# Optimization experiments

Hardware: AMD Instinct MI355X
Metric: run time of the kernel (lower is better)

The kernel has to match this reference:

```python
import jax, jax.numpy as jnp
import numpy as np

TOP_K = 4


def setup_inputs() -> dict:
    key = jax.random.key(0)
    ks = jax.random.split(key, 6)
    B, S, H, I, E = 2, 2048, 2880, 2880, 8
    scale = 0.02
    return {
        "x": jax.random.normal(ks[0], (B, S, H), dtype=jnp.float32),
        "router_w": jax.random.normal(ks[1], (E, H), dtype=jnp.float32) * scale,
        "router_b": jax.random.normal(ks[2], (E,), dtype=jnp.float32) * scale,
        "w_gate": jax.random.normal(ks[3], (E, H, I), dtype=jnp.float32) * scale,
        "w_up": jax.random.normal(ks[4], (E, H, I), dtype=jnp.float32) * scale,
        "w_down": jax.random.normal(ks[5], (E, I, H), dtype=jnp.float32) * scale,
    }


def _moe_forward(x, router_w, router_b, w_gate, w_up, w_down):
    B, S, H = x.shape
    E = router_w.shape[0]
    xf = x.reshape(-1, H)  # (T, H); note: self.norm is unused in the original forward
    T = xf.shape[0]

    # Router: linear -> top-k -> softmax over the k selected logits
    logits = xf @ router_w.T + router_b          # (T, E)
    topv, topi = jax.lax.top_k(logits, TOP_K)    # (T, K)
    aff_k = jax.nn.softmax(topv, axis=-1)        # (T, K), sums to 1
    aff = jnp.zeros_like(logits).at[jnp.arange(T)[:, None], topi].set(aff_k)  # (T, E)

    # Expert SwiGLU MLPs, affinity-weighted combine (aff is 0 for unselected experts)
    out = jnp.zeros_like(xf)
    for e in range(E):  # fixed small structural loop over experts
        g = xf @ w_gate[e]                       # (T, I)
        u = xf @ w_up[e]                         # (T, I)
        h = jax.nn.silu(g) * u                   # SwiGLU
        out = out + aff[:, e:e + 1] * (h @ w_down[e])
    return out.reshape(B, S, H)


def reference(x, router_w, router_b, w_gate, w_up, w_down):
    return _moe_forward(x, router_w, router_b, w_gate, w_up, w_down)
```

## Files before the change

### kernel.cpp

```cpp
#include <hip/hip_runtime.h>

#define T_TOK 4096
#define HDIM  2880
#define IDIM  2880
#define NEXP  8
#define TOPK  4
#define WEL   (2880 * 2880)

#define BM 128
#define BN 96
#define BK 64
#define NSTEP 45

typedef __attribute__((ext_vector_type(8))) short  s16x8;
typedef __attribute__((ext_vector_type(8))) unsigned short u16x8;
typedef __attribute__((ext_vector_type(4))) float  f32x4;

__device__ __forceinline__ unsigned short f2bf(float f) {
  unsigned int u = __float_as_uint(f);
  u += 0x7FFFu + ((u >> 16) & 1u);
  return (unsigned short)(u >> 16);
}

__device__ __forceinline__ void gload16(const unsigned short* g, unsigned short* l) {
  __builtin_amdgcn_global_load_lds(
      (const __attribute__((address_space(1))) void*)g,
      (__attribute__((address_space(3))) void*)l, 16, 0, 0);
}

__global__ __launch_bounds__(256) void cvt_kernel(const float* __restrict__ x,
                                                  unsigned short* __restrict__ xb) {
  int i = blockIdx.x * 256 + threadIdx.x;
  const f32x4* p = (const f32x4*)x;
  f32x4 a = p[2 * (size_t)i];
  f32x4 b = p[2 * (size_t)i + 1];
  u16x8 o;
  o[0] = f2bf(a[0]); o[1] = f2bf(a[1]); o[2] = f2bf(a[2]); o[3] = f2bf(a[3]);
  o[4] = f2bf(b[0]); o[5] = f2bf(b[1]); o[6] = f2bf(b[2]); o[7] = f2bf(b[3]);
  *(u16x8*)(xb + (size_t)i * 8) = o;
}

__global__ __launch_bounds__(256) void transpose_group_kernel(
    const float* __restrict__ wg, const float* __restrict__ wu,
    const float* __restrict__ wd, unsigned short* __restrict__ wbuf, int ge) {
  __shared__ unsigned short st[64][72];
  const int z = blockIdx.z, j = z / 3, m = z % 3;
  const float* src = (m == 0 ? wg : (m == 1 ? wu : wd)) + (size_t)(ge + j) * WEL;
  unsigned short* dst = wbuf + (size_t)(j * 3 + m) * WEL;
  const int k0 = blockIdx.x * 64, n0 = blockIdx.y * 64;
  const int tid = threadIdx.x;
#pragma unroll
  for (int u = 0; u < 4; ++u) {
    int idx = tid + u * 256;
    int kr = idx >> 4;
    int nc = (idx & 15) * 4;
    f32x4 v = *(const f32x4*)(src + (size_t)(k0 + kr) * 2880 + (n0 + nc));
#pragma unroll
    for (int q = 0; q < 4; ++q) st[nc + q][kr] = f2bf(v[q]);
  }
  __syncthreads();
  int n = tid >> 2;
  int kc = (tid & 3) * 16;
  u16x8 a = *(const u16x8*)(&st[n][kc]);
  u16x8 b = *(const u16x8*)(&st[n][kc + 8]);
  unsigned short* po = dst + (size_t)(n0 + n) * 2880 + (k0 + kc);
  *(u16x8*)(po) = a;
  *(u16x8*)(po + 8) = b;
}

__global__ __launch_bounds__(256) void router_kernel(const float* __restrict__ x,
                                                     const float* __restrict__ rw,
                                                     const float* __restrict__ rb,
                                                     float* __restrict__ aff,
                                                     int* __restrict__ cnt,
                                                     int* __restrict__ lst) {
  const int wv = threadIdx.x >> 6, lane = threadIdx.x & 63;
  const int tok0 = (blockIdx.x * 4 + wv) * 4;
  float acc[4][NEXP];
#pragma unroll
  for (int t = 0; t < 4; ++t)
#pragma unroll
    for (int e = 0; e < NEXP; ++e) acc[t][e] = 0.f;

#pragma unroll
  for (int it = 0; it < 12; ++it) {
    int c = it * 64 + lane;
    if (c < 720) {
      f32x4 w4[NEXP];
#pragma unroll
      for (int e = 0; e < NEXP; ++e)
        w4[e] = *(const f32x4*)(rw + (size_t)e * HDIM + c * 4);
#pragma unroll
      for (int t = 0; t < 4; ++t) {
        f32x4 xv = *(const f32x4*)(x + (size_t)(tok0 + t) * HDIM + c * 4);
#pragma unroll
        for (int e = 0; e < NEXP; ++e)
          acc[t][e] += xv[0] * w4[e][0] + xv[1] * w4[e][1] + xv[2] * w4[e][2] + xv[3] * w4[e][3];
      }
    }
  }
#pragma unroll
  for (int t = 0; t < 4; ++t)
#pragma unroll
    for (int e = 0; e < NEXP; ++e) {
#pragma unroll
      for (int m = 32; m; m >>= 1) acc[t][e] += __shfl_xor(acc[t][e], m);
    }
  if (lane < 4) {
    int tok = tok0 + lane;
    float lg[NEXP];
#pragma unroll
    for (int e = 0; e < NEXP; ++e) lg[e] = acc[lane][e] + rb[e];
    bool used[NEXP];
#pragma unroll
    for (int e = 0; e < NEXP; ++e) used[e] = false;
    int bi[TOPK]; float bv[TOPK];
#pragma unroll
    for (int s = 0; s < TOPK; ++s) {
      int best = 0; float vbest = -1e30f;
#pragma unroll
      for (int e = 0; e < NEXP; ++e)
        if (!used[e] && lg[e] > vbest) { vbest = lg[e]; best = e; }
      used[best] = true; bi[s] = best; bv[s] = vbest;
    }
    float mx = bv[0];
    float w[TOPK]; float ssum = 0.f;
#pragma unroll
    for (int s = 0; s < TOPK; ++s) { w[s] = __expf(bv[s] - mx); ssum += w[s]; }
    float o[NEXP];
#pragma unroll
    for (int e = 0; e < NEXP; ++e) o[e] = 0.f;
#pragma unroll
    for (int s = 0; s < TOPK; ++s) o[bi[s]] = w[s] / ssum;
#pragma unroll
    for (int e = 0; e < NEXP; ++e) aff[(size_t)tok * NEXP + e] = o[e];
#pragma unroll
    for (int s = 0; s < TOPK; ++s) {
      int p = atomicAdd(&cnt[bi[s]], 1);
      lst[bi[s] * T_TOK + p] = tok;
    }
  }
}

__global__ void sched_kernel(const int* __restrict__ cnt, int* __restrict__ ebs,
                             int* __restrict__ ess, int* __restrict__ gtot, int G) {
  if (threadIdx.x == 0 && blockIdx.x == 0) {
    int ng = NEXP / G;
    for (int g = 0; g < ng; ++g) {
      int b = 0, s = 0;
      for (int j = 0; j < G; ++j) {
        int e = g * G + j;
        ebs[e] = b; ess[e] = s;
        b += (cnt[e] + BM - 1) / BM;
        s += cnt[e];
      }
      gtot[g] = b;
    }
  }
}

__global__ __launch_bounds__(256) void gateup_kernel(
    const unsigned short* __restrict__ xb, const unsigned short* __restrict__ wbuf,
    const float* __restrict__ aff, const int* __restrict__ lst,
    const int* __restrict__ cnts, const int* __restrict__ ebs,
    const int* __restrict__ ess, const int* __restrict__ gtot_g,
    unsigned short* __restrict__ h4, int ge, int G) {
  const int bx = blockIdx.x;
  if (bx >= *gtot_g) return;
  int j = 0;
  for (int t = 1; t < G; ++t) j += (bx >= ebs[ge + t]) ? 1 : 0;
  const int e = ge + j;
  const int cnt = cnts[e];
  const int m0 = (bx - ebs[e]) * BM;
  const int slotbase = ess[e];
  const unsigned short* wgt = wbuf + (size_t)j * 3 * WEL;
  const unsigned short* wut = wgt + WEL;

  __shared__ __align__(16) unsigned short Al[BM * BK];
  __shared__ __align__(16) unsigned short Bgl[BN * BK];
  __shared__ __align__(16) unsigned short Bul[BN * BK];

  const int tid = threadIdx.x;
  const int n0 = blockIdx.y * BN;
  const int wv = tid >> 6, lane = tid & 63;
  const int msub = (wv >> 1) * 64, nsub = (wv & 1) * 48;
  const int l15 = lane & 15, l4 = lane >> 4;
  const int lr = lane >> 3, lc = lane & 7;
  const int* mylst = lst + e * T_TOK;

  const unsigned short* asrc[4]; unsigned short* adst[4];
#pragma unroll
  for (int u = 0; u < 4; ++u) {
    int s = u * 4 + wv;
    int r = s * 8 + lr;
    int tok = mylst[min(m0 + r, cnt - 1)];
    asrc[u] = xb + (size_t)tok * HDIM + (lc ^ (r & 7)) * 8;
    adst[u] = &Al[s * 512];
  }
  const unsigned short* bgsrc[3]; const unsigned short* busrc[3];
  unsigned short* bgdst[3]; unsigned short* budst[3];
#pragma unroll
  for (int u = 0; u < 3; ++u) {
    int s = u * 4 + wv;
    int r = s * 8 + lr;
    size_t off = (size_t)(n0 + r) * HDIM + (size_t)((lc ^ (r & 7)) * 8);
    bgsrc[u] = wgt + off; busrc[u] = wut + off;
    bgdst[u] = &Bgl[s * 512]; budst[u] = &Bul[s * 512];
  }

  f32x4 accg[4][3]; f32x4 accu[4][3];
#pragma unroll
  for (int mf = 0; mf < 4; ++mf)
#pragma unroll
    for (int nf = 0; nf < 3; ++nf) { accg[mf][nf] = (f32x4)0.f; accu[mf][nf] = (f32x4)0.f; }

#pragma unroll 1
  for (int k0 = 0; k0 < HDIM; k0 += BK) {
#pragma unroll
    for (int u = 0; u < 4; ++u) gload16(asrc[u] + k0, adst[u]);
#pragma unroll
    for (int u = 0; u < 3; ++u) {
      gload16(bgsrc[u] + k0, bgdst[u]);
      gload16(busrc[u] + k0, budst[u]);
    }
    __syncthreads();
#pragma unroll
    for (int kk = 0; kk < 2; ++kk) {
      s16x8 af[4];
#pragma unroll
      for (int mf = 0; mf < 4; ++mf) {
        int R = msub + mf * 16 + l15;
        int sl = (kk * 4 + l4) ^ (R & 7);
        af[mf] = *(const s16x8*)(&Al[R * 64 + sl * 8]);
      }
#pragma unroll
      for (int nf = 0; nf < 3; ++nf) {
        int R = nsub + nf * 16 + l15;
        int sl = (kk * 4 + l4) ^ (R & 7);
        s16x8 bg = *(const s16x8*)(&Bgl[R * 64 + sl * 8]);
        s16x8 bu = *(const s16x8*)(&Bul[R * 64 + sl * 8]);
#pragma unroll
        for (int mf = 0; mf < 4; ++mf) {
          accg[mf][nf] = __builtin_amdgcn_mfma_f32_16x16x32_bf16(af[mf], bg, accg[mf][nf], 0, 0, 0);
          accu[mf][nf] = __builtin_amdgcn_mfma_f32_16x16x32_bf16(af[mf], bu, accu[mf][nf], 0, 0, 0);
        }
      }
    }
    __syncthreads();
  }

#pragma unroll
  for (int mf = 0; mf < 4; ++mf)
#pragma unroll
    for (int r = 0; r < 4; ++r) {
      int slot = m0 + msub + mf * 16 + l4 * 4 + r;
      if (slot < cnt) {
        int tok = mylst[slot];
        float av = aff[(size_t)tok * NEXP + e];
#pragma unroll
        for (int nf = 0; nf < 3; ++nf) {
          float g = accg[mf][nf][r], uu = accu[mf][nf][r];
          float hv = (g / (1.f + __expf(-g))) * uu * av;
          int col = n0 + nsub + nf * 16 + l15;
          h4[(size_t)(slotbase + slot) * IDIM + col] = f2bf(hv);
        }
      }
    }
}

__global__ __launch_bounds__(256) void down_kernel(
    const unsigned short* __restrict__ h4, const unsigned short* __restrict__ wbuf,
    float* __restrict__ out, const int* __restrict__ lst,
    const int* __restrict__ cnts, const int* __restrict__ ebs,
    const int* __restrict__ ess, const int* __restrict__ gtot_g,
    int ge, int G) {
  const int bx = blockIdx.x;
  if (bx >= *gtot_g) return;
  int j = 0;
  for (int t = 1; t < G; ++t) j += (bx >= ebs[ge + t]) ? 1 : 0;
  const int e = ge + j;
  const int cnt = cnts[e];
  const int m0 = (bx - ebs[e]) * BM;
  const int slotbase = ess[e];
  const unsigned short* wdt = wbuf + (size_t)j * 3 * WEL + 2 * (size_t)WEL;

  __shared__ __align__(16) unsigned short Al[BM * BK];
  __shared__ __align__(16) unsigned short Bl[BN * BK];

  const int tid = threadIdx.x;
  const int n0 = blockIdx.y * BN;
  const int wv = tid >> 6, lane = tid & 63;
  const int msub = (wv >> 1) * 64, nsub = (wv & 1) * 48;
  const int l15 = lane & 15, l4 = lane >> 4;
  const int lr = lane >> 3, lc = lane & 7;
  const int* mylst = lst + e * T_TOK;

  const unsigned short* asrc[4]; unsigned short* adst[4];
#pragma unroll
  for (int u = 0; u < 4; ++u) {
    int s = u * 4 + wv;
    int r = s * 8 + lr;
    int hr = min(m0 + r, cnt - 1);
    asrc[u] = h4 + (size_t)(slotbase + hr) * IDIM + (lc ^ (r & 7)) * 8;
    adst[u] = &Al[s * 512];
  }
  const unsigned short* bsrc[3]; unsigned short* bdst[3];
#pragma unroll
  for (int u = 0; u < 3; ++u) {
    int s = u * 4 + wv;
    int r = s * 8 + lr;
    bsrc[u] = wdt + (size_t)(n0 + r) * IDIM + (size_t)((lc ^ (r & 7)) * 8);
    bdst[u] = &Bl[s * 512];
  }

  f32x4 acc[4][3];
#pragma unroll
  for (int mf = 0; mf < 4; ++mf)
#pragma unroll
    for (int nf = 0; nf < 3; ++nf) acc[mf][nf] = (f32x4)0.f;

#pragma unroll 1
  for (int k0 = 0; k0 < IDIM; k0 += BK) {
#pragma unroll
    for (int u = 0; u < 4; ++u) gload16(asrc[u] + k0, adst[u]);
#pragma unroll
    for (int u = 0; u < 3; ++u) gload16(bsrc[u] + k0, bdst[u]);
    __syncthreads();
#pragma unroll
    for (int kk = 0; kk < 2; ++kk) {
      s16x8 af[4];
#pragma unroll
      for (int mf = 0; mf < 4; ++mf) {
        int R = msub + mf * 16 + l15;
        int sl = (kk * 4 + l4) ^ (R & 7);
        af[mf] = *(const s16x8*)(&Al[R * 64 + sl * 8]);
      }
#pragma unroll
      for (int nf = 0; nf < 3; ++nf) {
        int R = nsub + nf * 16 + l15;
        int sl = (kk * 4 + l4) ^ (R & 7);
        s16x8 bb = *(const s16x8*)(&Bl[R * 64 + sl * 8]);
#pragma unroll
        for (int mf = 0; mf < 4; ++mf)
          acc[mf][nf] = __builtin_amdgcn_mfma_f32_16x16x32_bf16(af[mf], bb, acc[mf][nf], 0, 0, 0);
      }
    }
    __syncthreads();
  }

#pragma unroll
  for (int mf = 0; mf < 4; ++mf)
#pragma unroll
    for (int r = 0; r < 4; ++r) {
      int slot = m0 + msub + mf * 16 + l4 * 4 + r;
      if (slot < cnt) {
        int tok = mylst[slot];
#pragma unroll
        for (int nf = 0; nf < 3; ++nf) {
          int col = n0 + nsub + nf * 16 + l15;
          atomicAdd(out + (size_t)tok * HDIM + col, acc[mf][nf][r]);
        }
      }
    }
}

extern "C" void kernel_launch(void* const* d_in, const int* in_sizes, int n_in,
                              void* d_out, int out_size, void* d_ws, size_t ws_size,
                              hipStream_t stream) {
  (void)in_sizes; (void)n_in;
  const float* x  = (const float*)d_in[0];
  const float* rw = (const float*)d_in[1];
  const float* rb = (const float*)d_in[2];
  const float* wg = (const float*)d_in[3];
  const float* wu = (const float*)d_in[4];
  const float* wd = (const float*)d_in[5];
  float* out = (float*)d_out;

  char* ws = (char*)d_ws;
  float* aff = (float*)ws;
  int*   cnt = (int*)(ws + 131072);
  int*   lst = (int*)(ws + 131584);
  int*   ebs = (int*)(ws + 262656);
  int*   ess = (int*)(ws + 262720);
  int*   gtot = (int*)(ws + 262784);
  unsigned short* xb = (unsigned short*)(ws + 263168);
  const size_t OFF_H4 = 263168 + 23592960ull;

  const size_t WELB = (size_t)WEL * 2;
  int G = 1;
  {
    size_t need8 = OFF_H4 + (size_t)16384 * IDIM * 2 + 8 * 3 * WELB;
    size_t need2 = OFF_H4 + (size_t)8192  * IDIM * 2 + 2 * 3 * WELB;
    if (ws_size >= need8) G = 8;
    else if (ws_size >= need2) G = 2;
  }
  const size_t h4b = (size_t)((G == 8) ? 16384 : (G == 2 ? 8192 : 4096)) * IDIM * 2;
  unsigned short* h4   = (unsigned short*)(ws + OFF_H4);
  unsigned short* wbuf = (unsigned short*)(ws + OFF_H4 + h4b);

  const int NG = NEXP / G;
  const int GUX = (G == 8) ? 136 : (G == 2 ? 66 : 33);

  hipMemsetAsync(out, 0, (size_t)out_size * sizeof(float), stream);
  hipMemsetAsync(cnt, 0, 512, stream);
  cvt_kernel<<<(T_TOK * HDIM / 8) / 256, 256, 0, stream>>>(x, xb);
  router_kernel<<<T_TOK / 16, 256, 0, stream>>>(x, rw, rb, aff, cnt, lst);
  sched_kernel<<<1, 64, 0, stream>>>(cnt, ebs, ess, gtot, G);

  for (int g = 0; g < NG; ++g) {
    int ge = g * G;
    transpose_group_kernel<<<dim3(45, 45, 3 * G), 256, 0, stream>>>(wg, wu, wd, wbuf, ge);
    gateup_kernel<<<dim3(GUX, IDIM / BN), 256, 0, stream>>>(
        xb, wbuf, aff, lst, cnt, ebs, ess, gtot + g, h4, ge, G);
    down_kernel<<<dim3(GUX, HDIM / BN), 256, 0, stream>>>(
        h4, wbuf, out, lst, cnt, ebs, ess, gtot + g, ge, G);
  }
}
```

Before: 1.463 ms.

## Double-buffer LDS tiles in expert GEMMs and flatten grid to 1D panels

Both expert GEMM kernels now use two LDS buffers. The next K-tile's global-to-LDS loads are issued before computing on the current tile, with partial vmcnt waits instead of full syncthreads, so memory latency overlaps MFMA work. The 2D grid is also replaced by a 1D grid in which a block index maps to an (expert, m-tile, n-panel) triple, with m varying fastest inside each n panel. This is meant to compact out unused blocks and improve weight-panel reuse in cache. It doubles LDS use per block, which can lower occupancy, and it relies on hand-counted vmcnt values being correct.

```diff
diff --git a/kernel.cpp b/kernel.cpp
--- a/kernel.cpp
+++ b/kernel.cpp
@@ -10,6 +10,9 @@
 #define BM 128
 #define BN 96
 #define BK 64
+#define NPAN 30
+#define ASZ (BM * BK)
+#define BSZ (BN * BK)
 #define NSTEP 45
 
 typedef __attribute__((ext_vector_type(8))) short  s16x8;
@@ -142,7 +145,7 @@
   }
 }
 
-__global__ void sched_kernel(const int* __restrict__ cnt, int* __restrict__ ebs,
+__global__ void sched_kernel(const int* __restrict__ cnt, int* __restrict__ gbs,
                              int* __restrict__ ess, int* __restrict__ gtot, int G) {
   if (threadIdx.x == 0 && blockIdx.x == 0) {
     int ng = NEXP / G;
@@ -150,38 +153,50 @@
       int b = 0, s = 0;
       for (int j = 0; j < G; ++j) {
         int e = g * G + j;
-        ebs[e] = b; ess[e] = s;
-        b += (cnt[e] + BM - 1) / BM;
+        gbs[e] = b; ess[e] = s;
+        b += ((cnt[e] + BM - 1) / BM) * NPAN;
         s += cnt[e];
       }
       gtot[g] = b;
     }
   }
+}
+
+__device__ __forceinline__ bool locate(int bx, const int* gbs, const int* cnts,
+                                       int ge, int G, const int* gtot_g,
+                                       int& e, int& m0, int& n0, int& cnt) {
+  if (bx >= *gtot_g) return false;
+  int j = 0;
+  for (int t = 1; t < G; ++t) j += (bx >= gbs[ge + t]) ? 1 : 0;
+  e = ge + j;
+  cnt = cnts[e];
+  int mb = (cnt + BM - 1) >> 7;
+  int local = bx - gbs[e];
+  int nIdx = local / mb;
+  int mIdx = local - nIdx * mb;
+  m0 = mIdx * BM;
+  n0 = nIdx * BN;
+  return true;
 }
 
 __global__ __launch_bounds__(256) void gateup_kernel(
     const unsigned short* __restrict__ xb, const unsigned short* __restrict__ wbuf,
     const float* __restrict__ aff, const int* __restrict__ lst,
-    const int* __restrict__ cnts, const int* __restrict__ ebs,
+    const int* __restrict__ cnts, const int* __restrict__ gbs,
     const int* __restrict__ ess, const int* __restrict__ gtot_g,
     unsigned short* __restrict__ h4, int ge, int G) {
-  const int bx = blockIdx.x;
-  if (bx >= *gtot_g) return;
-  int j = 0;
-  for (int t = 1; t < G; ++t) j += (bx >= ebs[ge + t]) ? 1 : 0;
-  const int e = ge + j;
-  const int cnt = cnts[e];
-  const int m0 = (bx - ebs[e]) * BM;
+  int e, m0, n0, cnt;
+  if (!locate(blockIdx.x, gbs, cnts, ge, G, gtot_g, e, m0, n0, cnt)) return;
+  const int j = e - ge;
   const int slotbase = ess[e];
   const unsigned short* wgt = wbuf + (size_t)j * 3 * WEL;
   const unsigned short* wut = wgt + WEL;
 
-  __shared__ __align__(16) unsigned short Al[BM * BK];
-  __shared__ __align__(16) unsigned short Bgl[BN * BK];
-  __shared__ __align__(16) unsigned short Bul[BN * BK];
+  __shared__ __align__(16) unsigned short Al[2 * ASZ];
+  __shared__ __align__(16) unsigned short Bgl[2 * BSZ];
+  __shared__ __align__(16) unsigned short Bul[2 * BSZ];
 
   const int tid = threadIdx.x;
-  const int n0 = blockIdx.y * BN;
   const int wv = tid >> 6, lane = tid & 63;
   const int msub = (wv >> 1) * 64, nsub = (wv & 1) * 48;
   const int l15 = lane & 15, l4 = lane >> 4;
@@ -214,16 +229,20 @@
 #pragma unroll
     for (int nf = 0; nf < 3; ++nf) { accg[mf][nf] = (f32x4)0.f; accu[mf][nf] = (f32x4)0.f; }
 
-#pragma unroll 1
-  for (int k0 = 0; k0 < HDIM; k0 += BK) {
-#pragma unroll
-    for (int u = 0; u < 4; ++u) gload16(asrc[u] + k0, adst[u]);
+  auto stage = [&](int buf, int k0) {
+    int ao = buf * ASZ, bo = buf * BSZ;
+#pragma unroll
+    for (int u = 0; u < 4; ++u) gload16(asrc[u] + k0, adst[u] + ao);
 #pragma unroll
     for (int u = 0; u < 3; ++u) {
-      gload16(bgsrc[u] + k0, bgdst[u]);
-      gload16(busrc[u] + k0, budst[u]);
-    }
-    __syncthreads();
+      gload16(bgsrc[u] + k0, bgdst[u] + bo);
+      gload16(busrc[u] + k0, budst[u] + bo);
+    }
+  };
+  auto compute = [&](int buf) {
+    const unsigned short* Ab = Al + buf * ASZ;
+    const unsigned short* Bg = Bgl + buf * BSZ;
+    const unsigned short* Bu = Bul + buf * BSZ;
 #pragma unroll
     for (int kk = 0; kk < 2; ++kk) {
       s16x8 af[4];
@@ -231,14 +250,14 @@
       for (int mf = 0; mf < 4; ++mf) {
         int R = msub + mf * 16 + l15;
         int sl = (kk * 4 + l4) ^ (R & 7);
-        af[mf] = *(const s16x8*)(&Al[R * 64 + sl * 8]);
+        af[mf] = *(const s16x8*)(&Ab[R * 64 + sl * 8]);
       }
 #pragma unroll
       for (int nf = 0; nf < 3; ++nf) {
         int R = nsub + nf * 16 + l15;
         int sl = (kk * 4 + l4) ^ (R & 7);
-        s16x8 bg = *(const s16x8*)(&Bgl[R * 64 + sl * 8]);
-        s16x8 bu = *(const s16x8*)(&Bul[R * 64 + sl * 8]);
+        s16x8 bg = *(const s16x8*)(&Bg[R * 64 + sl * 8]);
+        s16x8 bu = *(const s16x8*)(&Bu[R * 64 + sl * 8]);
 #pragma unroll
         for (int mf = 0; mf < 4; ++mf) {
           accg[mf][nf] = __builtin_amdgcn_mfma_f32_16x16x32_bf16(af[mf], bg, accg[mf][nf], 0, 0, 0);
@@ -246,8 +265,25 @@
         }
       }
     }
-    __syncthreads();
-  }
+  };
+
+  stage(0, 0);
+#pragma unroll 1
+  for (int t = 0; t < NSTEP - 1; t += 2) {
+    stage(1, (t + 1) * BK);
+    asm volatile("s_waitcnt vmcnt(10)" ::: "memory");
+    __builtin_amdgcn_s_barrier();
+    compute(0);
+    __builtin_amdgcn_s_barrier();
+    stage(0, (t + 2) * BK);
+    asm volatile("s_waitcnt vmcnt(10)" ::: "memory");
+    __builtin_amdgcn_s_barrier();
+    compute(1);
+    __builtin_amdgcn_s_barrier();
+  }
+  asm volatile("s_waitcnt vmcnt(0)" ::: "memory");
+  __builtin_amdgcn_s_barrier();
+  compute(0);
 
 #pragma unroll
   for (int mf = 0; mf < 4; ++mf)
@@ -271,24 +307,19 @@
 __global__ __launch_bounds__(256) void down_kernel(
     const unsigned short* __restrict__ h4, const unsigned short* __restrict__ wbuf,
     float* __restrict__ out, const int* __restrict__ lst,
-    const int* __restrict__ cnts, const int* __restrict__ ebs,
+    const int* __restrict__ cnts, const int* __restrict__ gbs,
     const int* __restrict__ ess, const int* __restrict__ gtot_g,
     int ge, int G) {
-  const int bx = blockIdx.x;
-  if (bx >= *gtot_g) return;
-  int j = 0;
-  for (int t = 1; t < G; ++t) j += (bx >= ebs[ge + t]) ? 1 : 0;
-  const int e = ge + j;
-  const int cnt = cnts[e];
-  const int m0 = (bx - ebs[e]) * BM;
+  int e, m0, n0, cnt;
+  if (!locate(blockIdx.x, gbs, cnts, ge, G, gtot_g, e, m0, n0, cnt)) return;
+  const int j = e - ge;
   const int slotbase = ess[e];
   const unsigned short* wdt = wbuf + (size_t)j * 3 * WEL + 2 * (size_t)WEL;
 
-  __shared__ __align__(16) unsigned short Al[BM * BK];
-  __shared__ __align__(16) unsigned short Bl[BN * BK];
+  __shared__ __align__(16) unsigned short Al[2 * ASZ];
+  __shared__ __align__(16) unsigned short Bl[2 * BSZ];
 
   const int tid = threadIdx.x;
-  const int n0 = blockIdx.y * BN;
   const int wv = tid >> 6, lane = tid & 63;
   const int msub = (wv >> 1) * 64, nsub = (wv & 1) * 48;
   const int l15 = lane & 15, l4 = lane >> 4;
@@ -319,13 +350,16 @@
 #pragma unroll
     for (int nf = 0; nf < 3; ++nf) acc[mf][nf] = (f32x4)0.f;
 
-#pragma unroll 1
-  for (int k0 = 0; k0 < IDIM; k0 += BK) {
-#pragma unroll
-    for (int u = 0; u < 4; ++u) gload16(asrc[u] + k0, adst[u]);
-#pragma unroll
-    for (int u = 0; u < 3; ++u) gload16(bsrc[u] + k0, bdst[u]);
-    __syncthreads();
+  auto stage = [&](int buf, int k0) {
+    int ao = buf * ASZ, bo = buf * BSZ;
+#pragma unroll
+    for (int u = 0; u < 4; ++u) gload16(asrc[u] + k0, adst[u] + ao);
+#pragma unroll
+    for (int u = 0; u < 3; ++u) gload16(bsrc[u] + k0, bdst[u] + bo);
+  };
+  auto compute = [&](int buf) {
+    const unsigned short* Ab = Al + buf * ASZ;
+    const unsigned short* Bb = Bl + buf * BSZ;
 #pragma unroll
     for (int kk = 0; kk < 2; ++kk) {
       s16x8 af[4];
@@ -333,20 +367,37 @@
       for (int mf = 0; mf < 4; ++mf) {
         int R = msub + mf * 16 + l15;
         int sl = (kk * 4 + l4) ^ (R & 7);
-        af[mf] = *(const s16x8*)(&Al[R * 64 + sl * 8]);
+        af[mf] = *(const s16x8*)(&Ab[R * 64 + sl * 8]);
       }
 #pragma unroll
       for (int nf = 0; nf < 3; ++nf) {
         int R = nsub + nf * 16 + l15;
         int sl = (kk * 4 + l4) ^ (R & 7);
-        s16x8 bb = *(const s16x8*)(&Bl[R * 64 + sl * 8]);
+        s16x8 bb = *(const s16x8*)(&Bb[R * 64 + sl * 8]);
 #pragma unroll
         for (int mf = 0; mf < 4; ++mf)
           acc[mf][nf] = __builtin_amdgcn_mfma_f32_16x16x32_bf16(af[mf], bb, acc[mf][nf], 0, 0, 0);
       }
     }
-    __syncthreads();
-  }
+  };
+
+  stage(0, 0);
+#pragma unroll 1
+  for (int t = 0; t < NSTEP - 1; t += 2) {
+    stage(1, (t + 1) * BK);
+    asm volatile("s_waitcnt vmcnt(7)" ::: "memory");
+    __builtin_amdgcn_s_barrier();
+    compute(0);
+    __builtin_amdgcn_s_barrier();
+    stage(0, (t + 2) * BK);
+    asm volatile("s_waitcnt vmcnt(7)" ::: "memory");
+    __builtin_amdgcn_s_barrier();
+    compute(1);
+    __builtin_amdgcn_s_barrier();
+  }
+  asm volatile("s_waitcnt vmcnt(0)" ::: "memory");
+  __builtin_amdgcn_s_barrier();
+  compute(0);
 
 #pragma unroll
   for (int mf = 0; mf < 4; ++mf)
@@ -380,7 +431,7 @@
   float* aff = (float*)ws;
   int*   cnt = (int*)(ws + 131072);
   int*   lst = (int*)(ws + 131584);
-  int*   ebs = (int*)(ws + 262656);
+  int*   gbs = (int*)(ws + 262656);
   int*   ess = (int*)(ws + 262720);
   int*   gtot = (int*)(ws + 262784);
   unsigned short* xb = (unsigned short*)(ws + 263168);
@@ -399,20 +450,20 @@
   unsigned short* wbuf = (unsigned short*)(ws + OFF_H4 + h4b);
 
   const int NG = NEXP / G;
-  const int GUX = (G == 8) ? 136 : (G == 2 ? 66 : 33);
+  const int NBLK = (128 + G) * NPAN;
 
   hipMemsetAsync(out, 0, (size_t)out_size * sizeof(float), stream);
   hipMemsetAsync(cnt, 0, 512, stream);
   cvt_kernel<<<(T_TOK * HDIM / 8) / 256, 256, 0, stream>>>(x, xb);
   router_kernel<<<T_TOK / 16, 256, 0, stream>>>(x, rw, rb, aff, cnt, lst);
-  sched_kernel<<<1, 64, 0, stream>>>(cnt, ebs, ess, gtot, G);
+  sched_kernel<<<1, 64, 0, stream>>>(cnt, gbs, ess, gtot, G);
 
   for (int g = 0; g < NG; ++g) {
     int ge = g * G;
     transpose_group_kernel<<<dim3(45, 45, 3 * G), 256, 0, stream>>>(wg, wu, wd, wbuf, ge);
-    gateup_kernel<<<dim3(GUX, IDIM / BN), 256, 0, stream>>>(
-        xb, wbuf, aff, lst, cnt, ebs, ess, gtot + g, h4, ge, G);
-    down_kernel<<<dim3(GUX, HDIM / BN), 256, 0, stream>>>(
-        h4, wbuf, out, lst, cnt, ebs, ess, gtot + g, ge, G);
-  }
-}
+    gateup_kernel<<<NBLK, 256, 0, stream>>>(
+        xb, wbuf, aff, lst, cnt, gbs, ess, gtot + g, h4, ge, G);
+    down_kernel<<<NBLK, 256, 0, stream>>>(
+        h4, wbuf, out, lst, cnt, gbs, ess, gtot + g, ge, G);
+  }
+}
```

Result: faster. 1.410 ms (-3.6%).

## Double-buffer LDS with staged prefetch, 512-thread 256-row tiles, flattened XCD-swizzled grid

Applied to the files above, without the earlier changes.

Both expert GEMM kernels now use double-buffered LDS. Global-to-LDS prefetches for the next K step are split across barrier-separated MFMA phases, with s_setprio raised around the MFMA bursts. Tiles grow to 256 rows and 512 threads, the down kernel's N tile doubles to 192, and the 2D grid becomes a 1D flattened grid remapped through an XCD-aware swizzle so neighbouring tiles share L2. The goal is to hide load latency and improve operand reuse, at the cost of much more LDS and register use per block, lower occupancy, and a more fragile hand-written waitcnt schedule.

```diff
diff --git a/kernel.cpp b/kernel.cpp
--- a/kernel.cpp
+++ b/kernel.cpp
@@ -7,9 +7,15 @@
 #define TOPK  4
 #define WEL   (2880 * 2880)
 
-#define BM 128
-#define BN 96
+#define BM 256
+#define BN_GU 96
+#define BN_DN 192
 #define BK 64
+#define NPAN_GU 30
+#define NPAN_DN 15
+#define ASZ (BM * BK)
+#define BSZ_GU (BN_GU * BK)
+#define BSZ_DN (BN_DN * BK)
 #define NSTEP 45
 
 typedef __attribute__((ext_vector_type(8))) short  s16x8;
@@ -26,6 +32,12 @@
   __builtin_amdgcn_global_load_lds(
       (const __attribute__((address_space(1))) void*)g,
       (__attribute__((address_space(3))) void*)l, 16, 0, 0);
+}
+
+__device__ __forceinline__ int xcd_swz(int orig, int n) {
+  int q = n >> 3, r = n & 7;
+  int x = orig & 7, idx = orig >> 3;
+  return (x < r ? x * (q + 1) : r * (q + 1) + (x - r) * q) + idx;
 }
 
 __global__ __launch_bounds__(256) void cvt_kernel(const float* __restrict__ x,
@@ -142,46 +154,53 @@
   }
 }
 
-__global__ void sched_kernel(const int* __restrict__ cnt, int* __restrict__ ebs,
-                             int* __restrict__ ess, int* __restrict__ gtot, int G) {
+__global__ void sched_kernel(const int* __restrict__ cnt, int* __restrict__ gbs_gu,
+                             int* __restrict__ gbs_dn, int* __restrict__ ess,
+                             int* __restrict__ gtot_gu, int* __restrict__ gtot_dn, int G) {
   if (threadIdx.x == 0 && blockIdx.x == 0) {
     int ng = NEXP / G;
     for (int g = 0; g < ng; ++g) {
-      int b = 0, s = 0;
+      int bg_ = 0, bd_ = 0, s = 0;
       for (int j = 0; j < G; ++j) {
         int e = g * G + j;
-        ebs[e] = b; ess[e] = s;
-        b += (cnt[e] + BM - 1) / BM;
+        gbs_gu[e] = bg_; gbs_dn[e] = bd_; ess[e] = s;
+        int mb = (cnt[e] + BM - 1) / BM;
+        bg_ += mb * NPAN_GU;
+        bd_ += mb * NPAN_DN;
         s += cnt[e];
       }
-      gtot[g] = b;
-    }
-  }
-}
-
-__global__ __launch_bounds__(256) void gateup_kernel(
+      gtot_gu[g] = bg_; gtot_dn[g] = bd_;
+    }
+  }
+}
+
+__global__ __launch_bounds__(512) void gateup_kernel(
     const unsigned short* __restrict__ xb, const unsigned short* __restrict__ wbuf,
     const float* __restrict__ aff, const int* __restrict__ lst,
-    const int* __restrict__ cnts, const int* __restrict__ ebs,
+    const int* __restrict__ cnts, const int* __restrict__ gbs,
     const int* __restrict__ ess, const int* __restrict__ gtot_g,
     unsigned short* __restrict__ h4, int ge, int G) {
-  const int bx = blockIdx.x;
-  if (bx >= *gtot_g) return;
+  const int gt = *gtot_g;
+  if ((int)blockIdx.x >= gt) return;
+  const int bx = xcd_swz(blockIdx.x, gt);
   int j = 0;
-  for (int t = 1; t < G; ++t) j += (bx >= ebs[ge + t]) ? 1 : 0;
+  for (int t = 1; t < G; ++t) j += (bx >= gbs[ge + t]) ? 1 : 0;
   const int e = ge + j;
   const int cnt = cnts[e];
-  const int m0 = (bx - ebs[e]) * BM;
+  const int mb = (cnt + BM - 1) >> 8;
+  const int local = bx - gbs[e];
+  const int nIdx = local / mb;
+  const int m0 = (local - nIdx * mb) * BM;
+  const int n0 = nIdx * BN_GU;
   const int slotbase = ess[e];
   const unsigned short* wgt = wbuf + (size_t)j * 3 * WEL;
   const unsigned short* wut = wgt + WEL;
 
-  __shared__ __align__(16) unsigned short Al[BM * BK];
-  __shared__ __align__(16) unsigned short Bgl[BN * BK];
-  __shared__ __align__(16) unsigned short Bul[BN * BK];
+  __shared__ __align__(16) unsigned short Al[2 * ASZ];
+  __shared__ __align__(16) unsigned short Bgl[2 * BSZ_GU];
+  __shared__ __align__(16) unsigned short Bul[2 * BSZ_GU];
 
   const int tid = threadIdx.x;
-  const int n0 = blockIdx.y * BN;
   const int wv = tid >> 6, lane = tid & 63;
   const int msub = (wv >> 1) * 64, nsub = (wv & 1) * 48;
   const int l15 = lane & 15, l4 = lane >> 4;
@@ -191,21 +210,26 @@
   const unsigned short* asrc[4]; unsigned short* adst[4];
 #pragma unroll
   for (int u = 0; u < 4; ++u) {
-    int s = u * 4 + wv;
+    int s = wv + 8 * u;
     int r = s * 8 + lr;
     int tok = mylst[min(m0 + r, cnt - 1)];
     asrc[u] = xb + (size_t)tok * HDIM + (lc ^ (r & 7)) * 8;
     adst[u] = &Al[s * 512];
   }
-  const unsigned short* bgsrc[3]; const unsigned short* busrc[3];
-  unsigned short* bgdst[3]; unsigned short* budst[3];
-#pragma unroll
-  for (int u = 0; u < 3; ++u) {
-    int s = u * 4 + wv;
-    int r = s * 8 + lr;
-    size_t off = (size_t)(n0 + r) * HDIM + (size_t)((lc ^ (r & 7)) * 8);
-    bgsrc[u] = wgt + off; busrc[u] = wut + off;
-    bgdst[u] = &Bgl[s * 512]; budst[u] = &Bul[s * 512];
+  const unsigned short* bsrc[3]; unsigned short* bdst[3];
+  {
+    int r0 = wv * 8 + lr;
+    bsrc[0] = wgt + (size_t)(n0 + r0) * HDIM + (size_t)((lc ^ (r0 & 7)) * 8);
+    bdst[0] = &Bgl[wv * 512];
+    int s1 = (wv < 4) ? (8 + wv) : wv;
+    int r1 = s1 * 8 + lr;
+    size_t o1 = (size_t)(n0 + r1) * HDIM + (size_t)((lc ^ (r1 & 7)) * 8);
+    bsrc[1] = (wv < 4) ? (wgt + o1) : (wut + o1);
+    bdst[1] = (wv < 4) ? &Bgl[s1 * 512] : &Bul[s1 * 512];
+    int s2 = (wv < 4) ? wv : (4 + wv);
+    int r2 = s2 * 8 + lr;
+    bsrc[2] = wut + (size_t)(n0 + r2) * HDIM + (size_t)((lc ^ (r2 & 7)) * 8);
+    bdst[2] = &Bul[s2 * 512];
   }
 
   f32x4 accg[4][3]; f32x4 accu[4][3];
@@ -214,39 +238,89 @@
 #pragma unroll
     for (int nf = 0; nf < 3; ++nf) { accg[mf][nf] = (f32x4)0.f; accu[mf][nf] = (f32x4)0.f; }
 
+  gload16(asrc[0], adst[0]); gload16(asrc[1], adst[1]); gload16(asrc[2], adst[2]);
+  gload16(asrc[3], adst[3]);
+  gload16(bsrc[0], bdst[0]); gload16(bsrc[1], bdst[1]); gload16(bsrc[2], bdst[2]);
+
 #pragma unroll 1
-  for (int k0 = 0; k0 < HDIM; k0 += BK) {
-#pragma unroll
-    for (int u = 0; u < 4; ++u) gload16(asrc[u] + k0, adst[u]);
-#pragma unroll
-    for (int u = 0; u < 3; ++u) {
-      gload16(bgsrc[u] + k0, bgdst[u]);
-      gload16(busrc[u] + k0, budst[u]);
-    }
-    __syncthreads();
-#pragma unroll
-    for (int kk = 0; kk < 2; ++kk) {
-      s16x8 af[4];
-#pragma unroll
-      for (int mf = 0; mf < 4; ++mf) {
-        int R = msub + mf * 16 + l15;
-        int sl = (kk * 4 + l4) ^ (R & 7);
-        af[mf] = *(const s16x8*)(&Al[R * 64 + sl * 8]);
-      }
-#pragma unroll
-      for (int nf = 0; nf < 3; ++nf) {
-        int R = nsub + nf * 16 + l15;
-        int sl = (kk * 4 + l4) ^ (R & 7);
-        s16x8 bg = *(const s16x8*)(&Bgl[R * 64 + sl * 8]);
-        s16x8 bu = *(const s16x8*)(&Bul[R * 64 + sl * 8]);
-#pragma unroll
-        for (int mf = 0; mf < 4; ++mf) {
-          accg[mf][nf] = __builtin_amdgcn_mfma_f32_16x16x32_bf16(af[mf], bg, accg[mf][nf], 0, 0, 0);
-          accu[mf][nf] = __builtin_amdgcn_mfma_f32_16x16x32_bf16(af[mf], bu, accu[mf][nf], 0, 0, 0);
-        }
-      }
-    }
-    __syncthreads();
+  for (int t = 0; t < NSTEP; ++t) {
+    const int buf = t & 1, nb = buf ^ 1;
+    const int k1 = (t + 1) * BK;
+    const unsigned short* Ab = Al + buf * ASZ;
+    const unsigned short* Bg = Bgl + buf * BSZ_GU;
+    const unsigned short* Bu = Bul + buf * BSZ_GU;
+    if (t + 1 < NSTEP) {
+      gload16(asrc[0] + k1, adst[0] + nb * ASZ);
+      gload16(asrc[1] + k1, adst[1] + nb * ASZ);
+      gload16(asrc[2] + k1, adst[2] + nb * ASZ);
+      asm volatile("s_waitcnt vmcnt(3)" ::: "memory");
+    } else {
+      asm volatile("s_waitcnt vmcnt(0)" ::: "memory");
+    }
+    __builtin_amdgcn_s_barrier();
+    s16x8 af[4];
+#pragma unroll
+    for (int mf = 0; mf < 4; ++mf) {
+      int R = msub + mf * 16 + l15;
+      af[mf] = *(const s16x8*)(&Ab[R * 64 + (l4 ^ (R & 7)) * 8]);
+    }
+    __builtin_amdgcn_s_setprio(1);
+#pragma unroll
+    for (int nf = 0; nf < 3; ++nf) {
+      int R = nsub + nf * 16 + l15;
+      s16x8 b = *(const s16x8*)(&Bg[R * 64 + (l4 ^ (R & 7)) * 8]);
+#pragma unroll
+      for (int mf = 0; mf < 4; ++mf)
+        accg[mf][nf] = __builtin_amdgcn_mfma_f32_16x16x32_bf16(af[mf], b, accg[mf][nf], 0, 0, 0);
+    }
+    __builtin_amdgcn_s_setprio(0);
+    if (t + 1 < NSTEP) {
+      gload16(asrc[3] + k1, adst[3] + nb * ASZ);
+      gload16(bsrc[0] + k1, bdst[0] + nb * BSZ_GU);
+    }
+    __builtin_amdgcn_s_barrier();
+    __builtin_amdgcn_s_setprio(1);
+#pragma unroll
+    for (int nf = 0; nf < 3; ++nf) {
+      int R = nsub + nf * 16 + l15;
+      s16x8 b = *(const s16x8*)(&Bu[R * 64 + (l4 ^ (R & 7)) * 8]);
+#pragma unroll
+      for (int mf = 0; mf < 4; ++mf)
+        accu[mf][nf] = __builtin_amdgcn_mfma_f32_16x16x32_bf16(af[mf], b, accu[mf][nf], 0, 0, 0);
+    }
+    __builtin_amdgcn_s_setprio(0);
+    if (t + 1 < NSTEP) {
+      gload16(bsrc[1] + k1, bdst[1] + nb * BSZ_GU);
+      gload16(bsrc[2] + k1, bdst[2] + nb * BSZ_GU);
+    }
+    __builtin_amdgcn_s_barrier();
+#pragma unroll
+    for (int mf = 0; mf < 4; ++mf) {
+      int R = msub + mf * 16 + l15;
+      af[mf] = *(const s16x8*)(&Ab[R * 64 + ((4 + l4) ^ (R & 7)) * 8]);
+    }
+    __builtin_amdgcn_s_setprio(1);
+#pragma unroll
+    for (int nf = 0; nf < 3; ++nf) {
+      int R = nsub + nf * 16 + l15;
+      s16x8 b = *(const s16x8*)(&Bg[R * 64 + ((4 + l4) ^ (R & 7)) * 8]);
+#pragma unroll
+      for (int mf = 0; mf < 4; ++mf)
+        accg[mf][nf] = __builtin_amdgcn_mfma_f32_16x16x32_bf16(af[mf], b, accg[mf][nf], 0, 0, 0);
+    }
+    __builtin_amdgcn_s_setprio(0);
+    __builtin_amdgcn_s_barrier();
+    __builtin_amdgcn_s_setprio(1);
+#pragma unroll
+    for (int nf = 0; nf < 3; ++nf) {
+      int R = nsub + nf * 16 + l15;
+      s16x8 b = *(const s16x8*)(&Bu[R * 64 + ((4 + l4) ^ (R & 7)) * 8]);
+#pragma unroll
+      for (int mf = 0; mf < 4; ++mf)
+        accu[mf][nf] = __builtin_amdgcn_mfma_f32_16x16x32_bf16(af[mf], b, accu[mf][nf], 0, 0, 0);
+    }
+    __builtin_amdgcn_s_setprio(0);
+    __builtin_amdgcn_s_barrier();
   }
 
 #pragma unroll
@@ -268,29 +342,33 @@
     }
 }
 
-__global__ __launch_bounds__(256) void down_kernel(
+__global__ __launch_bounds__(512) void down_kernel(
     const unsigned short* __restrict__ h4, const unsigned short* __restrict__ wbuf,
     float* __restrict__ out, const int* __restrict__ lst,
-    const int* __restrict__ cnts, const int* __restrict__ ebs,
+    const int* __restrict__ cnts, const int* __restrict__ gbs,
     const int* __restrict__ ess, const int* __restrict__ gtot_g,
     int ge, int G) {
-  const int bx = blockIdx.x;
-  if (bx >= *gtot_g) return;
+  const int gt = *gtot_g;
+  if ((int)blockIdx.x >= gt) return;
+  const int bx = xcd_swz(blockIdx.x, gt);
   int j = 0;
-  for (int t = 1; t < G; ++t) j += (bx >= ebs[ge + t]) ? 1 : 0;
+  for (int t = 1; t < G; ++t) j += (bx >= gbs[ge + t]) ? 1 : 0;
   const int e = ge + j;
   const int cnt = cnts[e];
-  const int m0 = (bx - ebs[e]) * BM;
+  const int mb = (cnt + BM - 1) >> 8;
+  const int local = bx - gbs[e];
+  const int nIdx = local / mb;
+  const int m0 = (local - nIdx * mb) * BM;
+  const int n0 = nIdx * BN_DN;
   const int slotbase = ess[e];
   const unsigned short* wdt = wbuf + (size_t)j * 3 * WEL + 2 * (size_t)WEL;
 
-  __shared__ __align__(16) unsigned short Al[BM * BK];
-  __shared__ __align__(16) unsigned short Bl[BN * BK];
+  __shared__ __align__(16) unsigned short Al[2 * ASZ];
+  __shared__ __align__(16) unsigned short Bl[2 * BSZ_DN];
 
   const int tid = threadIdx.x;
-  const int n0 = blockIdx.y * BN;
   const int wv = tid >> 6, lane = tid & 63;
-  const int msub = (wv >> 1) * 64, nsub = (wv & 1) * 48;
+  const int msub = (wv >> 1) * 64, nsub = (wv & 1) * 96;
   const int l15 = lane & 15, l4 = lane >> 4;
   const int lr = lane >> 3, lc = lane & 7;
   const int* mylst = lst + e * T_TOK;
@@ -298,7 +376,7 @@
   const unsigned short* asrc[4]; unsigned short* adst[4];
 #pragma unroll
   for (int u = 0; u < 4; ++u) {
-    int s = u * 4 + wv;
+    int s = wv + 8 * u;
     int r = s * 8 + lr;
     int hr = min(m0 + r, cnt - 1);
     asrc[u] = h4 + (size_t)(slotbase + hr) * IDIM + (lc ^ (r & 7)) * 8;
@@ -306,46 +384,101 @@
   }
   const unsigned short* bsrc[3]; unsigned short* bdst[3];
 #pragma unroll
-  for (int u = 0; u < 3; ++u) {
-    int s = u * 4 + wv;
+  for (int v = 0; v < 3; ++v) {
+    int s = wv + 8 * v;
     int r = s * 8 + lr;
-    bsrc[u] = wdt + (size_t)(n0 + r) * IDIM + (size_t)((lc ^ (r & 7)) * 8);
-    bdst[u] = &Bl[s * 512];
-  }
-
-  f32x4 acc[4][3];
+    bsrc[v] = wdt + (size_t)(n0 + r) * IDIM + (size_t)((lc ^ (r & 7)) * 8);
+    bdst[v] = &Bl[s * 512];
+  }
+
+  f32x4 acc[4][6];
 #pragma unroll
   for (int mf = 0; mf < 4; ++mf)
 #pragma unroll
-    for (int nf = 0; nf < 3; ++nf) acc[mf][nf] = (f32x4)0.f;
+    for (int nf = 0; nf < 6; ++nf) acc[mf][nf] = (f32x4)0.f;
+
+  gload16(asrc[0], adst[0]); gload16(asrc[1], adst[1]); gload16(asrc[2], adst[2]);
+  gload16(asrc[3], adst[3]);
+  gload16(bsrc[0], bdst[0]); gload16(bsrc[1], bdst[1]); gload16(bsrc[2], bdst[2]);
 
 #pragma unroll 1
-  for (int k0 = 0; k0 < IDIM; k0 += BK) {
-#pragma unroll
-    for (int u = 0; u < 4; ++u) gload16(asrc[u] + k0, adst[u]);
-#pragma unroll
-    for (int u = 0; u < 3; ++u) gload16(bsrc[u] + k0, bdst[u]);
-    __syncthreads();
-#pragma unroll
-    for (int kk = 0; kk < 2; ++kk) {
-      s16x8 af[4];
-#pragma unroll
-      for (int mf = 0; mf < 4; ++mf) {
-        int R = msub + mf * 16 + l15;
-        int sl = (kk * 4 + l4) ^ (R & 7);
-        af[mf] = *(const s16x8*)(&Al[R * 64 + sl * 8]);
-      }
-#pragma unroll
-      for (int nf = 0; nf < 3; ++nf) {
-        int R = nsub + nf * 16 + l15;
-        int sl = (kk * 4 + l4) ^ (R & 7);
-        s16x8 bb = *(const s16x8*)(&Bl[R * 64 + sl * 8]);
-#pragma unroll
-        for (int mf = 0; mf < 4; ++mf)
-          acc[mf][nf] = __builtin_amdgcn_mfma_f32_16x16x32_bf16(af[mf], bb, acc[mf][nf], 0, 0, 0);
-      }
-    }
-    __syncthreads();
+  for (int t = 0; t < NSTEP; ++t) {
+    const int buf = t & 1, nb = buf ^ 1;
+    const int k1 = (t + 1) * BK;
+    const unsigned short* Ab = Al + buf * ASZ;
+    const unsigned short* Bb = Bl + buf * BSZ_DN;
+    if (t + 1 < NSTEP) {
+      gload16(asrc[0] + k1, adst[0] + nb * ASZ);
+      gload16(asrc[1] + k1, adst[1] + nb * ASZ);
+      gload16(asrc[2] + k1, adst[2] + nb * ASZ);
+      asm volatile("s_waitcnt vmcnt(3)" ::: "memory");
+    } else {
+      asm volatile("s_waitcnt vmcnt(0)" ::: "memory");
+    }
+    __builtin_amdgcn_s_barrier();
+    s16x8 af[4];
+#pragma unroll
+    for (int mf = 0; mf < 4; ++mf) {
+      int R = msub + mf * 16 + l15;
+      af[mf] = *(const s16x8*)(&Ab[R * 64 + (l4 ^ (R & 7)) * 8]);
+    }
+    __builtin_amdgcn_s_setprio(1);
+#pragma unroll
+    for (int nf = 0; nf < 3; ++nf) {
+      int R = nsub + nf * 16 + l15;
+      s16x8 b = *(const s16x8*)(&Bb[R * 64 + (l4 ^ (R & 7)) * 8]);
+#pragma unroll
+      for (int mf = 0; mf < 4; ++mf)
+        acc[mf][nf] = __builtin_amdgcn_mfma_f32_16x16x32_bf16(af[mf], b, acc[mf][nf], 0, 0, 0);
+    }
+    __builtin_amdgcn_s_setprio(0);
+    if (t + 1 < NSTEP) {
+      gload16(asrc[3] + k1, adst[3] + nb * ASZ);
+      gload16(bsrc[0] + k1, bdst[0] + nb * BSZ_DN);
+    }
+    __builtin_amdgcn_s_barrier();
+    __builtin_amdgcn_s_setprio(1);
+#pragma unroll
+    for (int nf = 3; nf < 6; ++nf) {
+      int R = nsub + nf * 16 + l15;
+      s16x8 b = *(const s16x8*)(&Bb[R * 64 + (l4 ^ (R & 7)) * 8]);
+#pragma unroll
+      for (int mf = 0; mf < 4; ++mf)
+        acc[mf][nf] = __builtin_amdgcn_mfma_f32_16x16x32_bf16(af[mf], b, acc[mf][nf], 0, 0, 0);
+    }
+    __builtin_amdgcn_s_setprio(0);
+    if (t + 1 < NSTEP) {
+      gload16(bsrc[1] + k1, bdst[1] + nb * BSZ_DN);
+      gload16(bsrc[2] + k1, bdst[2] + nb * BSZ_DN);
+    }
+    __builtin_amdgcn_s_barrier();
+#pragma unroll
+    for (int mf = 0; mf < 4; ++mf) {
+      int R = msub + mf * 16 + l15;
+      af[mf] = *(const s16x8*)(&Ab[R * 64 + ((4 + l4) ^ (R & 7)) * 8]);
+    }
+    __builtin_amdgcn_s_setprio(1);
+#pragma unroll
+    for (int nf = 0; nf < 3; ++nf) {
+      int R = nsub + nf * 16 + l15;
+      s16x8 b = *(const s16x8*)(&Bb[R * 64 + ((4 + l4) ^ (R & 7)) * 8]);
+#pragma unroll
+      for (int mf = 0; mf < 4; ++mf)
+        acc[mf][nf] = __builtin_amdgcn_mfma_f32_16x16x32_bf16(af[mf], b, acc[mf][nf], 0, 0, 0);
+    }
+    __builtin_amdgcn_s_setprio(0);
+    __builtin_amdgcn_s_barrier();
+    __builtin_amdgcn_s_setprio(1);
+#pragma unroll
+    for (int nf = 3; nf < 6; ++nf) {
+      int R = nsub + nf * 16 + l15;
+      s16x8 b = *(const s16x8*)(&Bb[R * 64 + ((4 + l4) ^ (R & 7)) * 8]);
+#pragma unroll
+      for (int mf = 0; mf < 4; ++mf)
+        acc[mf][nf] = __builtin_amdgcn_mfma_f32_16x16x32_bf16(af[mf], b, acc[mf][nf], 0, 0, 0);
+    }
+    __builtin_amdgcn_s_setprio(0);
+    __builtin_amdgcn_s_barrier();
   }
 
 #pragma unroll
@@ -356,7 +489,7 @@
       if (slot < cnt) {
         int tok = mylst[slot];
 #pragma unroll
-        for (int nf = 0; nf < 3; ++nf) {
+        for (int nf = 0; nf < 6; ++nf) {
           int col = n0 + nsub + nf * 16 + l15;
           atomicAdd(out + (size_t)tok * HDIM + col, acc[mf][nf][r]);
         }
@@ -377,12 +510,14 @@
   float* out = (float*)d_out;
 
   char* ws = (char*)d_ws;
-  float* aff = (float*)ws;
-  int*   cnt = (int*)(ws + 131072);
-  int*   lst = (int*)(ws + 131584);
-  int*   ebs = (int*)(ws + 262656);
-  int*   ess = (int*)(ws + 262720);
-  int*   gtot = (int*)(ws + 262784);
+  float* aff     = (float*)ws;
+  int*   cnt     = (int*)(ws + 131072);
+  int*   lst     = (int*)(ws + 131584);
+  int*   gbs_gu  = (int*)(ws + 262656);
+  int*   gbs_dn  = (int*)(ws + 262720);
+  int*   ess     = (int*)(ws + 262784);
+  int*   gtot_gu = (int*)(ws + 262848);
+  int*   gtot_dn = (int*)(ws + 262912);
   unsigned short* xb = (unsigned short*)(ws + 263168);
   const size_t OFF_H4 = 263168 + 23592960ull;
 
@@ -399,20 +534,21 @@
   unsigned short* wbuf = (unsigned short*)(ws + OFF_H4 + h4b);
 
   const int NG = NEXP / G;
-  const int GUX = (G == 8) ? 136 : (G == 2 ? 66 : 33);
+  const int NBLK_GU = (T_TOK * TOPK / BM + NEXP) * NPAN_GU;
+  const int NBLK_DN = (T_TOK * TOPK / BM + NEXP) * NPAN_DN;
 
   hipMemsetAsync(out, 0, (size_t)out_size * sizeof(float), stream);
   hipMemsetAsync(cnt, 0, 512, stream);
   cvt_kernel<<<(T_TOK * HDIM / 8) / 256, 256, 0, stream>>>(x, xb);
   router_kernel<<<T_TOK / 16, 256, 0, stream>>>(x, rw, rb, aff, cnt, lst);
-  sched_kernel<<<1, 64, 0, stream>>>(cnt, ebs, ess, gtot, G);
+  sched_kernel<<<1, 64, 0, stream>>>(cnt, gbs_gu, gbs_dn, ess, gtot_gu, gtot_dn, G);
 
   for (int g = 0; g < NG; ++g) {
     int ge = g * G;
     transpose_group_kernel<<<dim3(45, 45, 3 * G), 256, 0, stream>>>(wg, wu, wd, wbuf, ge);
-    gateup_kernel<<<dim3(GUX, IDIM / BN), 256, 0, stream>>>(
-        xb, wbuf, aff, lst, cnt, ebs, ess, gtot + g, h4, ge, G);
-    down_kernel<<<dim3(GUX, HDIM / BN), 256, 0, stream>>>(
-        h4, wbuf, out, lst, cnt, ebs, ess, gtot + g, ge, G);
-  }
-}
+    gateup_kernel<<<NBLK_GU, 512, 0, stream>>>(
+        xb, wbuf, aff, lst, cnt, gbs_gu, ess, gtot_gu + g, h4, ge, G);
+    down_kernel<<<NBLK_DN, 512, 0, stream>>>(
+        h4, wbuf, out, lst, cnt, gbs_dn, ess, gtot_dn + g, ge, G);
+  }
+}
```

New measurement: 1.624 ms. 1.11x slower.
